# Kernel tuning notes

Measured on AMD Instinct MI355X. Metric: run time of the kernel, lower is better.

Reference implementation:

```python
import jax, jax.numpy as jnp
import numpy as np

B, T, D = 64, 1024, 512
H, O = 512, 128
HALF = D // 2
ALPHA_M = 0.8


def setup_inputs() -> dict:
    key = jax.random.key(0)
    ks = jax.random.split(key, 6)
    s_in = 1.0 / np.sqrt(HALF)
    s_h = 1.0 / np.sqrt(H)
    return {
        "x": jax.random.normal(ks[0], (B, T, D), dtype=jnp.float32),
        "w1": jax.random.uniform(ks[1], (H, HALF), jnp.float32, -s_in, s_in),
        "b1": jnp.zeros((H,), jnp.float32),
        "tau1": jnp.full((H,), 3.0, jnp.float32),
        "w2": jax.random.uniform(ks[2], (H, HALF), jnp.float32, -s_in, s_in),
        "b2": jnp.zeros((H,), jnp.float32),
        "tau2": jnp.full((H,), 0.5, jnp.float32),
        "wo": jax.random.uniform(ks[3], (O, H), jnp.float32, -s_h, s_h),
        "bo": jnp.zeros((O,), jnp.float32),
    }


def reference(x, w1, b1, tau1, w2, b2, tau2, wo, bo):
    # Hoist the per-timestep branch Linears into two batched GEMMs.
    d1_in = jnp.einsum("bti,hi->tbh", x[:, :, :HALF], w1) + b1  # [T,B,H]
    d2_in = jnp.einsum("bti,hi->tbh", x[:, :, HALF:], w2) + b2  # [T,B,H]

    a1 = jax.nn.sigmoid(tau1)  # [H]
    a2 = jax.nn.sigmoid(tau2)  # [H]

    def step(carry, ins):
        d1, d2, mem = carry
        i1, i2 = ins
        d1 = a1 * d1 + (1.0 - a1) * i1
        d2 = a2 * d2 + (1.0 - a2) * i2
        mem = ALPHA_M * mem + (1.0 - ALPHA_M) * (d1 + d2)
        return (d1, d2, mem), mem

    z = jnp.zeros((x.shape[0], tau1.shape[0]), x.dtype)
    _, mems = jax.lax.scan(step, (z, z, z), (d1_in, d2_in))  # mems: [T,B,H]

    # Output projection + sigmoid, vectorized over all timesteps.
    out = jax.nn.sigmoid(jnp.einsum("tbh,oh->bto", mems, wo) + bo)  # [B,T,O]
    return out
```

## Files before the change

kernel.cpp:

```cpp
#include <hip/hip_runtime.h>


#define B_    64
#define T_    1024
#define D_    512
#define H_    512
#define O_    128
#define HALF_ 256
#define CLEN  32
#define NC    32

typedef __attribute__((ext_vector_type(4))) float        f32x4;
typedef __attribute__((ext_vector_type(2))) float        f32x2;
typedef __attribute__((ext_vector_type(8))) short        s16x8;
typedef __attribute__((ext_vector_type(4))) unsigned int u32x4;
typedef __attribute__((ext_vector_type(2))) unsigned int u32x2;

__device__ __forceinline__ unsigned short f2bf(float f) {
    unsigned u = __float_as_uint(f);
    return (unsigned short)((u + 0x7fffu + ((u >> 16) & 1u)) >> 16);
}
__device__ __forceinline__ unsigned packbf(float a, float b) {
    return (unsigned)f2bf(a) | ((unsigned)f2bf(b) << 16);
}
__device__ __forceinline__ float bflo(unsigned u) { return __uint_as_float(u << 16); }
__device__ __forceinline__ float bfu16(unsigned short u) {
    return __uint_as_float(((unsigned)u) << 16);
}
__device__ __forceinline__ float bfhi(unsigned u) { return __uint_as_float(u & 0xffff0000u); }
__device__ __forceinline__ float sigf(float x) { return 1.f / (1.f + __expf(-x)); }
__device__ __forceinline__ float guard(float dn) {
    if (fabsf(dn) < 1e-6f) dn = (dn < 0.f ? -1e-6f : 1e-6f);
    return dn;
}
__device__ __forceinline__ float pw32(float a) {
    float t = a * a; t *= t; t *= t; t *= t; t *= t; return t;
}

typedef const __attribute__((address_space(1))) unsigned int gu32;
typedef __attribute__((address_space(3))) unsigned int      lu32;
__device__ __forceinline__ void gl_lds16(const void* g, void* l) {
    __builtin_amdgcn_global_load_lds((gu32*)g, (lu32*)l, 16, 0, 0);
}

__global__ __launch_bounds__(256) void gtab_kernel(
    const float* __restrict__ tau1, const float* __restrict__ tau2,
    float* __restrict__ G1, float* __restrict__ G2)
{
    const int h = blockIdx.x * 256 + threadIdx.x;
    const float a1 = sigf(tau1[h]), a2 = sigf(tau2[h]);
    const float c1 = 0.2f * a1 / guard(0.8f - a1);
    const float c2 = 0.2f * a2 / guard(0.8f - a2);
    float pm = 1.f, p1 = 1.f, p2 = 1.f;
    for (int k = 0; k < CLEN; ++k) {
        pm *= 0.8f; p1 *= a1; p2 *= a2;
        G1[k * H_ + h] = c1 * (pm - p1);
        G2[k * H_ + h] = c2 * (pm - p2);
    }
}

__global__ __launch_bounds__(256) void wcast_kernel(
    const float* __restrict__ w1, const float* __restrict__ w2,
    const float* __restrict__ wo,
    unsigned int* __restrict__ w1b, unsigned int* __restrict__ w2b,
    unsigned int* __restrict__ wob)
{
    const float* s; unsigned int* d; int n;
    if (blockIdx.y == 0)      { s = w1; d = w1b; n = H_ * HALF_; }
    else if (blockIdx.y == 1) { s = w2; d = w2b; n = H_ * HALF_; }
    else                      { s = wo; d = wob; n = O_ * H_;    }
    int i = (blockIdx.x * 256 + threadIdx.x) * 4;
    if (i >= n) return;
    f32x4 a = *(const f32x4*)(s + i);
    u32x2 p;
    p.x = packbf(a.x, a.y);
    p.y = packbf(a.z, a.w);
    *(u32x2*)(d + i / 2) = p;
}

__global__ __launch_bounds__(256) void cast_kernel(const float* __restrict__ x,
                                                   unsigned int* __restrict__ xb) {
    size_t i = ((size_t)blockIdx.x * 256 + threadIdx.x) * 8;
    f32x4 a = *(const f32x4*)(x + i);
    f32x4 b = *(const f32x4*)(x + i + 4);
    u32x4 p;
    p.x = packbf(a.x, a.y); p.y = packbf(a.z, a.w);
    p.z = packbf(b.x, b.y); p.w = packbf(b.z, b.w);
    *(u32x4*)(xb + i / 2) = p;
}

__global__ __launch_bounds__(512, 4) void gemm1f_kernel(
    const unsigned short* __restrict__ xb,
    const unsigned short* __restrict__ w1b, const unsigned short* __restrict__ w2b,
    const float* __restrict__ b1, const float* __restrict__ tau1,
    const float* __restrict__ b2, const float* __restrict__ tau2,
    unsigned int* __restrict__ mems,
    float* __restrict__ Sd1, float* __restrict__ Sd2, float* __restrict__ Sm)
{
    __shared__ short smem[32768];
    short* As1 = smem;
    short* As2 = smem + 8192;
    short* Bs1 = smem + 16384;
    short* Bs2 = smem + 24576;
    short* d1L = smem;
    short* d2L = smem + 16384;

    const int nt = blockIdx.x;
    const int mt = blockIdx.y;
    const int b  = mt >> 3;
    const int t0 = (mt & 7) << 7;

    const int tid = threadIdx.x, l = tid & 63, wv = tid >> 6;
    const int ln = l & 15, qd = l >> 4;
    const int wm = (wv & 1) << 6;
    const int wn = (wv >> 1) << 5;

    const unsigned short* abase  = xb + (size_t)(mt * 128) * D_;
    const unsigned short* w1base = w1b + (size_t)(nt * 128) * HALF_;
    const unsigned short* w2base = w2b + (size_t)(nt * 128) * HALF_;

    f32x4 acc0[4][2] = {};
    f32x4 acc1[4][2] = {};

    for (int kt = 0; kt < HALF_; kt += 64) {
        #pragma unroll
        for (int i = 0; i < 2; ++i) {
            int ch = wv * 2 + i;
            int r  = ch * 8 + (l >> 3);
            int kbl = (l & 7) ^ (r & 7);
            gl_lds16(abase + (size_t)r * D_ + kt + kbl * 8,         &As1[ch * 512 + l * 8]);
        }
        #pragma unroll
        for (int i = 0; i < 2; ++i) {
            int ch = wv * 2 + i;
            int r  = ch * 8 + (l >> 3);
            int kbl = (l & 7) ^ (r & 7);
            gl_lds16(abase + (size_t)r * D_ + HALF_ + kt + kbl * 8, &As2[ch * 512 + l * 8]);
        }
        #pragma unroll
        for (int i = 0; i < 2; ++i) {
            int ch = wv * 2 + i;
            int r  = ch * 8 + (l >> 3);
            int kbl = (l & 7) ^ (r & 7);
            gl_lds16(w1base + (size_t)r * HALF_ + kt + kbl * 8,     &Bs1[ch * 512 + l * 8]);
        }
        #pragma unroll
        for (int i = 0; i < 2; ++i) {
            int ch = wv * 2 + i;
            int r  = ch * 8 + (l >> 3);
            int kbl = (l & 7) ^ (r & 7);
            gl_lds16(w2base + (size_t)r * HALF_ + kt + kbl * 8,     &Bs2[ch * 512 + l * 8]);
        }
        __syncthreads();
        #pragma unroll
        for (int ks = 0; ks < 64; ks += 32) {
            s16x8 af[4], bfv[2];
            #pragma unroll
            for (int i = 0; i < 4; ++i) {
                int r = wm + i * 16 + ln;
                int kbp = ((ks >> 3) + qd) ^ (r & 7);
                af[i] = *(const s16x8*)&As1[r * 64 + kbp * 8];
            }
            #pragma unroll
            for (int j = 0; j < 2; ++j) {
                int r = wn + j * 16 + ln;
                int kbp = ((ks >> 3) + qd) ^ (r & 7);
                bfv[j] = *(const s16x8*)&Bs1[r * 64 + kbp * 8];
            }
            #pragma unroll
            for (int i = 0; i < 4; ++i)
                #pragma unroll
                for (int j = 0; j < 2; ++j)
                    acc0[i][j] = __builtin_amdgcn_mfma_f32_16x16x32_bf16(
                        af[i], bfv[j], acc0[i][j], 0, 0, 0);
            #pragma unroll
            for (int i = 0; i < 4; ++i) {
                int r = wm + i * 16 + ln;
                int kbp = ((ks >> 3) + qd) ^ (r & 7);
                af[i] = *(const s16x8*)&As2[r * 64 + kbp * 8];
            }
            #pragma unroll
            for (int j = 0; j < 2; ++j) {
                int r = wn + j * 16 + ln;
                int kbp = ((ks >> 3) + qd) ^ (r & 7);
                bfv[j] = *(const s16x8*)&Bs2[r * 64 + kbp * 8];
            }
            #pragma unroll
            for (int i = 0; i < 4; ++i)
                #pragma unroll
                for (int j = 0; j < 2; ++j)
                    acc1[i][j] = __builtin_amdgcn_mfma_f32_16x16x32_bf16(
                        af[i], bfv[j], acc1[i][j], 0, 0, 0);
        }
        __syncthreads();
    }

    #pragma unroll
    for (int i = 0; i < 4; ++i)
        #pragma unroll
        for (int j = 0; j < 2; ++j)
            #pragma unroll
            for (int r = 0; r < 4; ++r) {
                int t  = wm + i * 16 + qd * 4 + r;
                int hc = (wn + j * 16 + ln) ^ ((t & 12) << 2);
                d1L[t * 128 + hc] = (short)f2bf(acc0[i][j][r]);
                d2L[t * 128 + hc] = (short)f2bf(acc1[i][j][r]);
            }
    __syncthreads();

    const int cl = tid >> 7;
    const int h  = tid & 127;
    const int hg = nt * 128 + h;
    const int cg = ((mt & 7) << 2) + cl;

    const float a1 = sigf(tau1[hg]);
    const float a2 = sigf(tau2[hg]);
    const float o1 = 1.f - a1, o2 = 1.f - a2;
    const float bb1 = b1[hg], bb2 = b2[hg];

    float d1 = 0.f, d2 = 0.f, m = 0.f;
    unsigned short* msh = (unsigned short*)mems;
    const size_t mrow = (size_t)(b * T_ + t0 + cl * CLEN) * H_ + hg;

    #pragma unroll 8
    for (int k = 0; k < CLEN; ++k) {
        int t  = cl * CLEN + k;
        int hc = h ^ ((t & 12) << 2);
        float i1 = bfu16((unsigned short)d1L[t * 128 + hc]) + bb1;
        float i2 = bfu16((unsigned short)d2L[t * 128 + hc]) + bb2;
        d1 = a1 * d1 + o1 * i1;
        d2 = a2 * d2 + o2 * i2;
        m  = 0.8f * m + 0.2f * (d1 + d2);
        msh[mrow + (size_t)k * H_] = f2bf(m);
    }

    const size_t si = (size_t)(cg * B_ + b) * H_ + hg;
    Sd1[si] = d1;
    Sd2[si] = d2;
    Sm[si]  = m;
}

__global__ __launch_bounds__(128) void scanB_kernel(
    const float* __restrict__ Sd1, const float* __restrict__ Sd2,
    const float* __restrict__ Sm,
    const float* __restrict__ tau1, const float* __restrict__ tau2,
    float* __restrict__ D1, float* __restrict__ D2, float* __restrict__ DM)
{
    const int g = blockIdx.x * 128 + threadIdx.x;
    const int h2 = g & 255, b = g >> 8, h0 = h2 << 1;

    const float a1a = sigf(tau1[h0]), a1b = sigf(tau1[h0 + 1]);
    const float a2a = sigf(tau2[h0]), a2b = sigf(tau2[h0 + 1]);
    const float amL = pw32(0.8f);
    const float a1La = pw32(a1a), a1Lb = pw32(a1b);
    const float a2La = pw32(a2a), a2Lb = pw32(a2b);

    const float c1a = 0.2f * a1a / guard(0.8f - a1a);
    const float c1b = 0.2f * a1b / guard(0.8f - a1b);
    const float c2a = 0.2f * a2a / guard(0.8f - a2a);
    const float c2b = 0.2f * a2b / guard(0.8f - a2b);

    const float g1La = c1a * (amL - a1La), g1Lb = c1b * (amL - a1Lb);
    const float g2La = c2a * (amL - a2La), g2Lb = c2b * (amL - a2Lb);

    float D1a = 0.f, D1b = 0.f, D2a = 0.f, D2b = 0.f, Ma = 0.f, Mb = 0.f;
    for (int c = 0; c < NC; ++c) {
        const size_t si = (size_t)(c * B_ + b) * H_ + h0;
        f32x2 v;
        v.x = D1a; v.y = D1b; *(f32x2*)&D1[si] = v;
        v.x = D2a; v.y = D2b; *(f32x2*)&D2[si] = v;
        v.x = Ma;  v.y = Mb;  *(f32x2*)&DM[si] = v;
        f32x2 s1 = *(const f32x2*)&Sd1[si];
        f32x2 s2 = *(const f32x2*)&Sd2[si];
        f32x2 sm = *(const f32x2*)&Sm[si];
        float nMa = amL * Ma + D1a * g1La + D2a * g2La + sm.x;
        float nMb = amL * Mb + D1b * g1Lb + D2b * g2Lb + sm.y;
        D1a = a1La * D1a + s1.x;  D1b = a1Lb * D1b + s1.y;
        D2a = a2La * D2a + s2.x;  D2b = a2Lb * D2b + s2.y;
        Ma = nMa;  Mb = nMb;
    }
}

__global__ __launch_bounds__(512, 4) void gemm2f_kernel(
    const unsigned short* __restrict__ mems, const unsigned short* __restrict__ wob,
    const float* __restrict__ bo,
    const float* __restrict__ G1, const float* __restrict__ G2,
    const float* __restrict__ D1, const float* __restrict__ D2,
    const float* __restrict__ DM, float* __restrict__ out)
{
    __shared__ short As[128 * 64];
    __shared__ short Bs[128 * 64];
    __shared__ float PMl[CLEN];

    const int mt = blockIdx.x;
    const int b = mt >> 3, c0 = (mt & 7) << 2;
    const int tid = threadIdx.x, l = tid & 63, wv = tid >> 6;
    const int ln = l & 15, qd = l >> 4;
    const int wm = (wv & 1) << 6;
    const int wn = (wv >> 1) << 5;

    if (tid < CLEN) {
        float pm = 1.f;
        for (int k = 0; k <= tid; ++k) pm *= 0.8f;
        PMl[tid] = pm;
    }
    __syncthreads();

    f32x4 acc[4][2] = {};
    const unsigned short* abase = mems + (size_t)(mt * 128) * H_;

    for (int kt = 0; kt < H_; kt += 64) {
        #pragma unroll
        for (int i = 0; i < 2; ++i) {
            int ch = wv * 2 + i;
            int r  = ch * 8 + (l >> 3);
            int kbl = (l & 7) ^ (r & 7);
            gl_lds16(wob + (size_t)r * H_ + kt + kbl * 8, &Bs[ch * 512 + l * 8]);
        }
        #pragma unroll
        for (int i = 0; i < 2; ++i) {
            int gi = i * 512 + tid;
            int r = gi >> 3, kbp = gi & 7, kbl = kbp ^ (r & 7);
            int h0 = kt + kbl * 8;
            int k = r & 31, c = c0 + (r >> 5);
            size_t dbase = (size_t)(c * B_ + b) * H_ + h0;
            f32x4 d1a = *(const f32x4*)&D1[dbase], d1b = *(const f32x4*)&D1[dbase + 4];
            f32x4 d2a = *(const f32x4*)&D2[dbase], d2b = *(const f32x4*)&D2[dbase + 4];
            f32x4 dma = *(const f32x4*)&DM[dbase], dmb = *(const f32x4*)&DM[dbase + 4];
            f32x4 g1a = *(const f32x4*)&G1[k * H_ + h0], g1b = *(const f32x4*)&G1[k * H_ + h0 + 4];
            f32x4 g2a = *(const f32x4*)&G2[k * H_ + h0], g2b = *(const f32x4*)&G2[k * H_ + h0 + 4];
            float pm = PMl[k];
            u32x4 mv = *(const u32x4*)(abase + (size_t)r * H_ + h0);
            float v0 = bflo(mv.x) + d1a.x * g1a.x + d2a.x * g2a.x + dma.x * pm;
            float v1 = bfhi(mv.x) + d1a.y * g1a.y + d2a.y * g2a.y + dma.y * pm;
            float v2 = bflo(mv.y) + d1a.z * g1a.z + d2a.z * g2a.z + dma.z * pm;
            float v3 = bfhi(mv.y) + d1a.w * g1a.w + d2a.w * g2a.w + dma.w * pm;
            float v4 = bflo(mv.z) + d1b.x * g1b.x + d2b.x * g2b.x + dmb.x * pm;
            float v5 = bfhi(mv.z) + d1b.y * g1b.y + d2b.y * g2b.y + dmb.y * pm;
            float v6 = bflo(mv.w) + d1b.z * g1b.z + d2b.z * g2b.z + dmb.z * pm;
            float v7 = bfhi(mv.w) + d1b.w * g1b.w + d2b.w * g2b.w + dmb.w * pm;
            u32x4 p;
            p.x = packbf(v0, v1); p.y = packbf(v2, v3);
            p.z = packbf(v4, v5); p.w = packbf(v6, v7);
            *(u32x4*)&As[r * 64 + kbp * 8] = p;
        }
        __syncthreads();
        #pragma unroll
        for (int ks = 0; ks < 64; ks += 32) {
            s16x8 af[4], bfv[2];
            #pragma unroll
            for (int i = 0; i < 4; ++i) {
                int r = wm + i * 16 + ln;
                int kbp = ((ks >> 3) + qd) ^ (r & 7);
                af[i] = *(const s16x8*)&As[r * 64 + kbp * 8];
            }
            #pragma unroll
            for (int j = 0; j < 2; ++j) {
                int r = wn + j * 16 + ln;
                int kbp = ((ks >> 3) + qd) ^ (r & 7);
                bfv[j] = *(const s16x8*)&Bs[r * 64 + kbp * 8];
            }
            #pragma unroll
            for (int i = 0; i < 4; ++i)
                #pragma unroll
                for (int j = 0; j < 2; ++j)
                    acc[i][j] = __builtin_amdgcn_mfma_f32_16x16x32_bf16(
                        af[i], bfv[j], acc[i][j], 0, 0, 0);
        }
        __syncthreads();
    }

    float bov[2];
    #pragma unroll
    for (int j = 0; j < 2; ++j) bov[j] = bo[wn + j * 16 + ln];

    float* orow = out + (size_t)(mt * 128 + wm + qd * 4) * O_ + wn + ln;
    #pragma unroll
    for (int i = 0; i < 4; ++i)
        #pragma unroll
        for (int j = 0; j < 2; ++j)
            #pragma unroll
            for (int r = 0; r < 4; ++r) {
                float v = acc[i][j][r] + bov[j];
                orow[(size_t)(i * 16 + r) * O_ + j * 16] = 1.f / (1.f + __expf(-v));
            }
}

extern "C" void kernel_launch(void* const* d_in, const int* in_sizes, int n_in,
                              void* d_out, int out_size, void* d_ws, size_t ws_size,
                              hipStream_t stream) {
    const float* x    = (const float*)d_in[0];
    const float* w1   = (const float*)d_in[1];
    const float* b1   = (const float*)d_in[2];
    const float* tau1 = (const float*)d_in[3];
    const float* w2   = (const float*)d_in[4];
    const float* b2   = (const float*)d_in[5];
    const float* tau2 = (const float*)d_in[6];
    const float* wo   = (const float*)d_in[7];
    const float* bo   = (const float*)d_in[8];
    float* out = (float*)d_out;

    char* w = (char*)d_ws;
    unsigned short* xb   = (unsigned short*)(w);
    unsigned int*   mems = (unsigned int*)(w + (size_t)64 * 1024 * 1024);
    float* Sd1 = (float*)(w + (size_t)128 * 1024 * 1024);
    float* Sd2 = Sd1 + (1u << 20);
    float* Sm  = Sd1 + (2u << 20);
    float* D1  = Sd1 + (3u << 20);
    float* D2  = Sd1 + (4u << 20);
    float* DM  = Sd1 + (5u << 20);
    float* G1  = Sd1 + (6u << 20);
    float* G2  = G1 + CLEN * H_;
    unsigned short* w1b = (unsigned short*)(G2 + CLEN * H_);
    unsigned short* w2b = w1b + (size_t)H_ * HALF_;
    unsigned short* wob = w2b + (size_t)H_ * HALF_;

    gtab_kernel<<<dim3(2), 256, 0, stream>>>(tau1, tau2, G1, G2);
    wcast_kernel<<<dim3(128, 3), 256, 0, stream>>>(w1, w2, wo,
                                                   (unsigned int*)w1b,
                                                   (unsigned int*)w2b,
                                                   (unsigned int*)wob);
    cast_kernel<<<dim3(16384), 256, 0, stream>>>(x, (unsigned int*)xb);
    gemm1f_kernel<<<dim3(4, 512), 512, 0, stream>>>(xb, w1b, w2b, b1, tau1, b2, tau2,
                                                    mems, Sd1, Sd2, Sm);
    scanB_kernel<<<dim3(128), 128, 0, stream>>>(Sd1, Sd2, Sm, tau1, tau2, D1, D2, DM);
    gemm2f_kernel<<<dim3(512), 512, 0, stream>>>((const unsigned short*)mems, wob, bo,
                                                 G1, G2, D1, D2, DM, out);
}
```

Baseline: 353.4 us.

## Double-buffer gemm1 LDS tiles with K=32 steps and k-major layout

Replaces the single-buffered 64-wide K loop in the fused branch GEMM with a two-stage ping-pong LDS pipeline over 32-wide K slices. The next slice is prefetched while MFMAs run on the current one, and only one barrier is used per step. The LDS layout changes from a swizzled row-major tile to a k-block-major layout, which removes the XOR address math. The trade-off is more loop iterations and barriers, plus possible LDS bank conflicts from the unswizzled layout.

```diff
diff --git a/kernel.cpp b/kernel.cpp
--- a/kernel.cpp
+++ b/kernel.cpp
@@ -98,10 +98,6 @@
     float* __restrict__ Sd1, float* __restrict__ Sd2, float* __restrict__ Sm)
 {
     __shared__ short smem[32768];
-    short* As1 = smem;
-    short* As2 = smem + 8192;
-    short* Bs1 = smem + 16384;
-    short* Bs2 = smem + 24576;
     short* d1L = smem;
     short* d2L = smem + 16384;
 
@@ -119,53 +115,45 @@
     const unsigned short* w1base = w1b + (size_t)(nt * 128) * HALF_;
     const unsigned short* w2base = w2b + (size_t)(nt * 128) * HALF_;
 
+    const int kb = wv >> 1;
+    const int rr = ((wv & 1) << 6) + l;
+    const int dst = wv * 512 + l * 8;
+
     f32x4 acc0[4][2] = {};
     f32x4 acc1[4][2] = {};
 
-    for (int kt = 0; kt < HALF_; kt += 64) {
-        #pragma unroll
-        for (int i = 0; i < 2; ++i) {
-            int ch = wv * 2 + i;
-            int r  = ch * 8 + (l >> 3);
-            int kbl = (l & 7) ^ (r & 7);
-            gl_lds16(abase + (size_t)r * D_ + kt + kbl * 8,         &As1[ch * 512 + l * 8]);
+    {
+        short* base = smem;
+        gl_lds16(abase  + (size_t)rr * D_    + kb * 8,         base + dst);
+        gl_lds16(abase  + (size_t)rr * D_    + HALF_ + kb * 8, base + 4096  + dst);
+        gl_lds16(w1base + (size_t)rr * HALF_ + kb * 8,         base + 8192  + dst);
+        gl_lds16(w2base + (size_t)rr * HALF_ + kb * 8,         base + 12288 + dst);
+    }
+    asm volatile("s_waitcnt vmcnt(0)" ::: "memory");
+    __builtin_amdgcn_s_barrier();
+
+    int cur = 0;
+    for (int t = 0; t < 8; ++t) {
+        if (t < 7) {
+            short* nb = smem + (cur ^ 1) * 16384;
+            int kt = (t + 1) * 32;
+            gl_lds16(abase  + (size_t)rr * D_    + kt + kb * 8,         nb + dst);
+            gl_lds16(abase  + (size_t)rr * D_    + HALF_ + kt + kb * 8, nb + 4096  + dst);
+            gl_lds16(w1base + (size_t)rr * HALF_ + kt + kb * 8,         nb + 8192  + dst);
+            gl_lds16(w2base + (size_t)rr * HALF_ + kt + kb * 8,         nb + 12288 + dst);
         }
-        #pragma unroll
-        for (int i = 0; i < 2; ++i) {
-            int ch = wv * 2 + i;
-            int r  = ch * 8 + (l >> 3);
-            int kbl = (l & 7) ^ (r & 7);
-            gl_lds16(abase + (size_t)r * D_ + HALF_ + kt + kbl * 8, &As2[ch * 512 + l * 8]);
-        }
-        #pragma unroll
-        for (int i = 0; i < 2; ++i) {
-            int ch = wv * 2 + i;
-            int r  = ch * 8 + (l >> 3);
-            int kbl = (l & 7) ^ (r & 7);
-            gl_lds16(w1base + (size_t)r * HALF_ + kt + kbl * 8,     &Bs1[ch * 512 + l * 8]);
-        }
-        #pragma unroll
-        for (int i = 0; i < 2; ++i) {
-            int ch = wv * 2 + i;
-            int r  = ch * 8 + (l >> 3);
-            int kbl = (l & 7) ^ (r & 7);
-            gl_lds16(w2base + (size_t)r * HALF_ + kt + kbl * 8,     &Bs2[ch * 512 + l * 8]);
-        }
-        __syncthreads();
-        #pragma unroll
-        for (int ks = 0; ks < 64; ks += 32) {
+        {
+            short* base = smem + cur * 16384;
             s16x8 af[4], bfv[2];
             #pragma unroll
             for (int i = 0; i < 4; ++i) {
                 int r = wm + i * 16 + ln;
-                int kbp = ((ks >> 3) + qd) ^ (r & 7);
-                af[i] = *(const s16x8*)&As1[r * 64 + kbp * 8];
+                af[i] = *(const s16x8*)&base[qd * 1024 + r * 8];
             }
             #pragma unroll
             for (int j = 0; j < 2; ++j) {
                 int r = wn + j * 16 + ln;
-                int kbp = ((ks >> 3) + qd) ^ (r & 7);
-                bfv[j] = *(const s16x8*)&Bs1[r * 64 + kbp * 8];
+                bfv[j] = *(const s16x8*)&base[8192 + qd * 1024 + r * 8];
             }
             #pragma unroll
             for (int i = 0; i < 4; ++i)
@@ -176,14 +164,12 @@
             #pragma unroll
             for (int i = 0; i < 4; ++i) {
                 int r = wm + i * 16 + ln;
-                int kbp = ((ks >> 3) + qd) ^ (r & 7);
-                af[i] = *(const s16x8*)&As2[r * 64 + kbp * 8];
+                af[i] = *(const s16x8*)&base[4096 + qd * 1024 + r * 8];
             }
             #pragma unroll
             for (int j = 0; j < 2; ++j) {
                 int r = wn + j * 16 + ln;
-                int kbp = ((ks >> 3) + qd) ^ (r & 7);
-                bfv[j] = *(const s16x8*)&Bs2[r * 64 + kbp * 8];
+                bfv[j] = *(const s16x8*)&base[12288 + qd * 1024 + r * 8];
             }
             #pragma unroll
             for (int i = 0; i < 4; ++i)
@@ -192,7 +178,9 @@
                     acc1[i][j] = __builtin_amdgcn_mfma_f32_16x16x32_bf16(
                         af[i], bfv[j], acc1[i][j], 0, 0, 0);
         }
-        __syncthreads();
+        asm volatile("s_waitcnt vmcnt(0)" ::: "memory");
+        __builtin_amdgcn_s_barrier();
+        cur ^= 1;
     }
 
     #pragma unroll
```

After: 377.3 us. 1.07x slower.
